# Kernel optimization log

Measured on AMD Instinct MI355X. Metric: run time of the kernel, lower is better.

## Reference

```python
import jax, jax.numpy as jnp
import numpy as np
from functools import partial

B, DIN, H, D, HW = 4096, 2048, 1024, 256, 256
MAX_STEPS = 15
STEP = 1.0 / MAX_STEPS
WEIGHT = 1.0


def safe_norm(x):
    # per-sample L2 norm, keepdims, nan-safe at 0
    return jnp.sqrt(jnp.sum(x * x, axis=-1, keepdims=True) + 1e-24)


def setup_inputs() -> dict:
    key = jax.random.key(0)
    ks = jax.random.split(key, 16)
    s = lambda fan: 1.0 / np.sqrt(fan)
    inp = {
        'x_start': jax.random.normal(ks[0], (B, DIN), jnp.float32),
        'x_end': jax.random.normal(ks[1], (B, DIN), jnp.float32),
        'noise_raw': jax.random.normal(ks[2], (B, D), jnp.float32),
        # encoder params
        'W1': jax.random.normal(ks[3], (DIN, H), jnp.float32) * s(DIN),
        'b1': jnp.zeros((H,), jnp.float32),
        'W2': jax.random.normal(ks[4], (H, D), jnp.float32) * s(H),
        'b2': jnp.zeros((D,), jnp.float32),
        # Zermelo wind field params
        'Ww1': jax.random.normal(ks[5], (D, HW), jnp.float32) * s(D),
        'bw1': jnp.zeros((HW,), jnp.float32),
        'Ww2': jax.random.normal(ks[6], (HW, D), jnp.float32) * s(HW),
        'bw2': jnp.zeros((D,), jnp.float32),
        # conformal potential phi params (metric g = exp(phi) I)
        'Wp1': jax.random.normal(ks[7], (D, HW), jnp.float32) * s(D),
        'bp1': jnp.zeros((HW,), jnp.float32),
        'wp2': jax.random.normal(ks[8], (HW,), jnp.float32) * s(HW),
    }
    return inp


def _encode(x, W1, b1, W2, b2):
    return jnp.tanh(x @ W1 + b1) @ W2 + b2  # [B, D]


def _wind(z, Ww1, bw1, Ww2, bw2):
    return jnp.tanh(z @ Ww1 + bw1) @ Ww2 + bw2  # [B, D]


def _grad_phi(x, Wp1, bp1, wp2):
    # phi(x) = wp2 . tanh(x @ Wp1 + bp1); analytic gradient, fully vectorized
    h = jnp.tanh(x @ Wp1 + bp1)          # [B, HW]
    return ((1.0 - h * h) * wp2) @ Wp1.T  # [B, D]


def _accel(x, v, Wp1, bp1, wp2):
    # geodesic spray of conformal metric e^{phi} I:
    # a = -(grad_phi . v) v + 0.5 |v|^2 grad_phi
    g = _grad_phi(x, Wp1, bp1, wp2)
    gv = jnp.sum(g * v, axis=-1, keepdims=True)
    vv = jnp.sum(v * v, axis=-1, keepdims=True)
    return -gv * v + 0.5 * vv * g


def _trace(z0, v0, Wp1, bp1, wp2):
    h = STEP
    acc = partial(_accel, Wp1=Wp1, bp1=bp1, wp2=wp2)

    def step(carry, _):
        x, v = carry
        k1x, k1v = v, acc(x, v)
        k2x, k2v = v + 0.5 * h * k1v, acc(x + 0.5 * h * k1x, v + 0.5 * h * k1v)
        k3x, k3v = v + 0.5 * h * k2v, acc(x + 0.5 * h * k2x, v + 0.5 * h * k2v)
        k4x, k4v = v + h * k3v, acc(x + h * k3x, v + h * k3v)
        xn = x + (h / 6.0) * (k1x + 2 * k2x + 2 * k3x + k4x)
        vn = v + (h / 6.0) * (k1v + 2 * k2v + 2 * k3v + k4v)
        return (xn, vn), xn

    (_, _), xs = jax.lax.scan(step, (z0, v0), None, length=MAX_STEPS)
    return xs  # [MAX_STEPS, B, D] == xs[1:] of the original trace


def reference(x_start, x_end, noise_raw, W1, b1, W2, b2,
              Ww1, bw1, Ww2, bw2, Wp1, bp1, wp2):
    z_s = _encode(x_start, W1, b1, W2, b2)
    z_e = _encode(x_end, W1, b1, W2, b2)
    W_start = _wind(z_s, Ww1, bw1, Ww2, bw2)
    # degenerate-wind fallback: tiny tangent noise (Euclidean manifold -> identity projection)
    noise = noise_raw / (safe_norm(noise_raw) + 1e-12) * 1e-4
    w_norm = safe_norm(W_start)  # [B, 1]
    W_start = jnp.where(w_norm < 1e-5, W_start + noise, W_start)
    xs = _trace(z_s, W_start, Wp1, bp1, wp2)          # [S, B, D]
    dists_sq = jnp.sum((xs - z_e) ** 2, axis=-1)      # [S, B]
    min_dist_sq = jnp.min(dists_sq, axis=0)           # closest approach per sample
    return jnp.mean(min_dist_sq) * WEIGHT
```

## Files before the change

kernel.cpp:

```cpp
#include <hip/hip_runtime.h>
#include <math.h>

typedef short bf8 __attribute__((ext_vector_type(8)));
typedef float f32x4 __attribute__((ext_vector_type(4)));

namespace {

constexpr float H_STEP = 1.0f / 15.0f;

__device__ inline short f2bf(float f) {
  unsigned u = __float_as_uint(f);
  u += 0x7fffu + ((u >> 16) & 1u);
  return (short)(u >> 16);
}

__device__ inline float fast_tanh(float x) {
  const float ax = fabsf(x);
  const float e = __expf(-2.0f * ax);
  const float t = (1.0f - e) * __builtin_amdgcn_rcpf(1.0f + e);
  return copysignf(t, x);
}

__device__ inline float sech2(float x) {
  const float e = __expf(-2.0f * fabsf(x));
  const float r = __builtin_amdgcn_rcpf(1.0f + e);
  return 4.0f * e * r * r;
}

__device__ inline float wave_sum(float v) {
#pragma unroll
  for (int sh = 32; sh > 0; sh >>= 1) v += __shfl_xor(v, sh);
  return v;
}

template <int CTRL>
__device__ inline float dppadd(float v) {
  return v + __int_as_float(__builtin_amdgcn_update_dpp(
                 0, __float_as_int(v), CTRL, 0xF, 0xF, true));
}
__device__ inline float red16(float v) {
  v = dppadd<0x121>(v);
  v = dppadd<0x122>(v);
  v = dppadd<0x124>(v);
  v = dppadd<0x128>(v);
  return v;
}

__device__ inline void async16(const void* g, void* l) {
  __builtin_amdgcn_global_load_lds((__attribute__((address_space(1))) void*)g,
                                   (__attribute__((address_space(3))) void*)l,
                                   16, 0, 0);
}


__global__ __launch_bounds__(256) void cvt2(const float* __restrict__ a,
                                            const float* __restrict__ b,
                                            short* __restrict__ dst, long n) {
  const long half = n >> 1;
  long i = ((long)blockIdx.x * 256 + threadIdx.x) * 4;
  const long stride = (long)gridDim.x * 1024;
  for (; i < n; i += stride) {
    const float* s = (i < half) ? (a + i) : (b + (i - half));
    const float4 f = *(const float4*)s;
    ushort4 o;
    o.x = (unsigned short)f2bf(f.x);
    o.y = (unsigned short)f2bf(f.y);
    o.z = (unsigned short)f2bf(f.z);
    o.w = (unsigned short)f2bf(f.w);
    *(ushort4*)(dst + i) = o;
  }
}

__global__ __launch_bounds__(256) void cvt_w(
    const float* __restrict__ W1, const float* __restrict__ W2,
    const float* __restrict__ Ww1, const float* __restrict__ Ww2,
    const float* __restrict__ Wp1, const float* __restrict__ wp2,
    short* __restrict__ W1T, short* __restrict__ W2T,
    short* __restrict__ Ww1T, short* __restrict__ Ww2T,
    short* __restrict__ WpT, short* __restrict__ Wp1s) {
  __shared__ float tile[32][33];
  const int id = blockIdx.x;
  const int tr = threadIdx.x >> 5, tc = threadIdx.x & 31;
  const float* src;
  short* dst;
  int K, N, kt, nt;
  if (id < 2048) {
    src = W1; dst = W1T; K = 2048; N = 1024; kt = id >> 5; nt = id & 31;
  } else if (id < 2304) {
    src = W2; dst = W2T; K = 1024; N = 256; kt = (id - 2048) >> 3; nt = (id - 2048) & 7;
  } else if (id < 2368) {
    src = Ww1; dst = Ww1T; K = 256; N = 256; kt = (id - 2304) >> 3; nt = (id - 2304) & 7;
  } else if (id < 2432) {
    src = Ww2; dst = Ww2T; K = 256; N = 256; kt = (id - 2368) >> 3; nt = (id - 2368) & 7;
  } else if (id < 2496) {
    src = Wp1; dst = WpT; K = 256; N = 256; kt = (id - 2432) >> 3; nt = (id - 2432) & 7;
  } else {
    const int lid = id - 2496;
    const int k0 = (lid >> 3) * 32, n0 = (lid & 7) * 32;
#pragma unroll
    for (int i = 0; i < 32; i += 8) {
      const size_t o = (size_t)(k0 + tr + i) * 256 + n0 + tc;
      Wp1s[o] = f2bf(Wp1[o] * wp2[n0 + tc]);
    }
    return;
  }
  const int k0 = kt * 32, n0 = nt * 32;
#pragma unroll
  for (int i = 0; i < 32; i += 8)
    tile[tr + i][tc] = src[(size_t)(k0 + tr + i) * N + n0 + tc];
  __syncthreads();
#pragma unroll
  for (int i = 0; i < 32; i += 8)
    dst[(size_t)(n0 + tr + i) * K + k0 + tc] = f2bf(tile[tc][tr + i]);
}


__global__ __launch_bounds__(256) void gemm128_tanh(
    const short* __restrict__ A, const short* __restrict__ Bt,
    const float* __restrict__ bias, short* __restrict__ Cb, int M, int N,
    int K) {
  __shared__ __align__(16) short As[2 * 128 * 32];
  __shared__ __align__(16) short Bs[2 * 128 * 32];
  const int tid = threadIdx.x;
  const int w = tid >> 6, lane = tid & 63, q = lane >> 4, l15 = lane & 15;
  const int wm = (w >> 1) * 64, wn = (w & 1) * 64;
  const int m0 = blockIdx.y * 128, n0 = blockIdx.x * 128;
  const f32x4 fzero = {0.0f, 0.0f, 0.0f, 0.0f};
  f32x4 acc[4][4];
#pragma unroll
  for (int mt = 0; mt < 4; ++mt)
#pragma unroll
    for (int nt = 0; nt < 4; ++nt) acc[mt][nt] = fzero;

  for (int k0 = 0; k0 < K; k0 += 64) {
#pragma unroll
    for (int kcb = 0; kcb < 2; ++kcb)
#pragma unroll
      for (int j = 0; j < 2; ++j) {
        const int c = w * 128 + j * 64 + lane;
        async16(A + (size_t)(m0 + (c >> 2)) * K + k0 + kcb * 32 + (c & 3) * 8,
                &As[kcb * 4096 + (w * 128 + j * 64) * 8]);
        async16(Bt + (size_t)(n0 + (c >> 2)) * K + k0 + kcb * 32 + (c & 3) * 8,
                &Bs[kcb * 4096 + (w * 128 + j * 64) * 8]);
      }
    __syncthreads();
#pragma unroll
    for (int kcb = 0; kcb < 2; ++kcb) {
      bf8 af[4], bfr[4];
#pragma unroll
      for (int mt = 0; mt < 4; ++mt)
        af[mt] =
            *(const bf8*)&As[kcb * 4096 + (wm + mt * 16 + l15) * 32 + q * 8];
#pragma unroll
      for (int nt = 0; nt < 4; ++nt)
        bfr[nt] =
            *(const bf8*)&Bs[kcb * 4096 + (wn + nt * 16 + l15) * 32 + q * 8];
#pragma unroll
      for (int mt = 0; mt < 4; ++mt)
#pragma unroll
        for (int nt = 0; nt < 4; ++nt)
          acc[mt][nt] = __builtin_amdgcn_mfma_f32_16x16x32_bf16(
              af[mt], bfr[nt], acc[mt][nt], 0, 0, 0);
    }
    __syncthreads();
  }
#pragma unroll
  for (int mt = 0; mt < 4; ++mt)
#pragma unroll
    for (int nt = 0; nt < 4; ++nt) {
      const int col = n0 + wn + nt * 16 + l15;
      const float bcol = bias[col];
#pragma unroll
      for (int rg = 0; rg < 4; ++rg) {
        const int row = m0 + wm + mt * 16 + q * 4 + rg;
        Cb[(size_t)row * N + col] = f2bf(fast_tanh(acc[mt][nt][rg] + bcol));
      }
    }
}

__global__ __launch_bounds__(256) void gemm64_enc2(
    const short* __restrict__ A, const short* __restrict__ Bt,
    const float* __restrict__ bias, float* __restrict__ Zs,
    float* __restrict__ Ze, int M, int N, int K) {
  __shared__ __align__(16) short As[64 * 32];
  __shared__ __align__(16) short Bs[64 * 32];
  const int tid = threadIdx.x;
  const int w = tid >> 6, lane = tid & 63, q = lane >> 4, l15 = lane & 15;
  const int wm = (w >> 1) * 32, wn = (w & 1) * 32;
  const int m0 = blockIdx.y * 64, n0 = blockIdx.x * 64;
  const f32x4 fzero = {0.0f, 0.0f, 0.0f, 0.0f};
  f32x4 acc[2][2];
#pragma unroll
  for (int mt = 0; mt < 2; ++mt)
#pragma unroll
    for (int nt = 0; nt < 2; ++nt) acc[mt][nt] = fzero;

  for (int k0 = 0; k0 < K; k0 += 32) {
    const int c = w * 64 + lane;
    async16(A + (size_t)(m0 + (c >> 2)) * K + k0 + (c & 3) * 8,
            &As[(w * 64) * 8]);
    async16(Bt + (size_t)(n0 + (c >> 2)) * K + k0 + (c & 3) * 8,
            &Bs[(w * 64) * 8]);
    __syncthreads();
    bf8 af[2], bfr[2];
#pragma unroll
    for (int mt = 0; mt < 2; ++mt)
      af[mt] = *(const bf8*)&As[(wm + mt * 16 + l15) * 32 + q * 8];
#pragma unroll
    for (int nt = 0; nt < 2; ++nt)
      bfr[nt] = *(const bf8*)&Bs[(wn + nt * 16 + l15) * 32 + q * 8];
#pragma unroll
    for (int mt = 0; mt < 2; ++mt)
#pragma unroll
      for (int nt = 0; nt < 2; ++nt)
        acc[mt][nt] = __builtin_amdgcn_mfma_f32_16x16x32_bf16(
            af[mt], bfr[nt], acc[mt][nt], 0, 0, 0);
    __syncthreads();
  }
#pragma unroll
  for (int mt = 0; mt < 2; ++mt)
#pragma unroll
    for (int nt = 0; nt < 2; ++nt) {
      const int col = n0 + wn + nt * 16 + l15;
      const float bcol = bias[col];
#pragma unroll
      for (int rg = 0; rg < 4; ++rg) {
        const int row = m0 + wm + mt * 16 + q * 4 + rg;
        const float val = acc[mt][nt][rg] + bcol;
        if (row < 4096)
          Zs[(size_t)row * N + col] = val;
        else
          Ze[(size_t)(row - 4096) * N + col] = val;
      }
    }
}


__global__ __launch_bounds__(512, 2) void trace_fused(
    const float* __restrict__ Xg, const float* __restrict__ ZEg,
    const float* __restrict__ NZg, const short* __restrict__ WT,
    const short* __restrict__ Wp1s, const short* __restrict__ Ww1T,
    const short* __restrict__ Ww2T, const float* __restrict__ bw1,
    const float* __restrict__ bw2, const float* __restrict__ bp1,
    float* __restrict__ out) {
  constexpr float hs = H_STEP;
  __shared__ __align__(16) short XsL[4096];
  __shared__ __align__(16) short UL[4096];
  __shared__ __align__(16) float gvb[2][16];
  __shared__ __align__(16) float vvb[2][16];
  __shared__ __align__(16) float db[2][16];
  const int tid = threadIdx.x;
  const int w = tid >> 6, lane = tid & 63, q = lane >> 4, l15 = lane & 15;
  const int r0 = blockIdx.x * 16, rb = q * 4;

  if (tid < 16) {
    gvb[0][tid] = 0.0f; gvb[1][tid] = 0.0f;
    vvb[0][tid] = 0.0f; vvb[1][tid] = 0.0f;
    db[0][tid] = 0.0f;  db[1][tid] = 0.0f;
  }

  int cc[2], wadr[2][4], radr[8];
  float bp1c[2], bw1c[2], bw2c[2];
#pragma unroll
  for (int t = 0; t < 2; ++t) {
    const int c = w * 32 + t * 16 + l15;
    cc[t] = c;
    const int kc = c >> 3, cx = kc & 15, cl = c & 7;
#pragma unroll
    for (int rg = 0; rg < 4; ++rg)
      wadr[t][rg] = kc * 128 + ((rb + rg) ^ cx) * 8 + cl;
    bp1c[t] = bp1[c];
    bw1c[t] = bw1[c];
    bw2c[t] = bw2[c];
  }
#pragma unroll
  for (int ks = 0; ks < 8; ++ks) {
    const int kq = ks * 4 + q;
    radr[ks] = (kq * 16 + (l15 ^ (kq & 15))) * 8;
  }
  float x[2][4], ze[2][4], nz[2][4];
#pragma unroll
  for (int t = 0; t < 2; ++t)
#pragma unroll
    for (int rg = 0; rg < 4; ++rg) {
      const size_t off = (size_t)(r0 + rb + rg) * 256 + cc[t];
      x[t][rg] = Xg[off];
      ze[t][rg] = ZEg[off];
      nz[t][rg] = NZg[off];
    }
  const f32x4 fzero = {0.0f, 0.0f, 0.0f, 0.0f};

  float v[2][4];
  {
    bf8 Wf1[2][8], Wf2[2][8];
#pragma unroll
    for (int t = 0; t < 2; ++t)
#pragma unroll
      for (int ks = 0; ks < 8; ++ks) {
        Wf1[t][ks] = *(const bf8*)(Ww1T + cc[t] * 256 + ks * 32 + q * 8);
        Wf2[t][ks] = *(const bf8*)(Ww2T + cc[t] * 256 + ks * 32 + q * 8);
      }
#pragma unroll
    for (int t = 0; t < 2; ++t)
#pragma unroll
      for (int rg = 0; rg < 4; ++rg) XsL[wadr[t][rg]] = f2bf(x[t][rg]);
    __syncthreads();
    bf8 af[8];
#pragma unroll
    for (int ks = 0; ks < 8; ++ks) af[ks] = *(const bf8*)&XsL[radr[ks]];
    f32x4 acc[2];
#pragma unroll
    for (int t = 0; t < 2; ++t) {
      f32x4 a0 = fzero, a1 = fzero;
#pragma unroll
      for (int ks = 0; ks < 8; ks += 2) {
        a0 = __builtin_amdgcn_mfma_f32_16x16x32_bf16(af[ks], Wf1[t][ks], a0,
                                                     0, 0, 0);
        a1 = __builtin_amdgcn_mfma_f32_16x16x32_bf16(af[ks + 1],
                                                     Wf1[t][ks + 1], a1, 0, 0,
                                                     0);
      }
      acc[t] = a0 + a1;
    }
#pragma unroll
    for (int t = 0; t < 2; ++t)
#pragma unroll
      for (int rg = 0; rg < 4; ++rg)
        UL[wadr[t][rg]] = f2bf(fast_tanh(acc[t][rg] + bw1c[t]));
    __syncthreads();
#pragma unroll
    for (int ks = 0; ks < 8; ++ks) af[ks] = *(const bf8*)&UL[radr[ks]];
#pragma unroll
    for (int t = 0; t < 2; ++t) {
      f32x4 a0 = fzero, a1 = fzero;
#pragma unroll
      for (int ks = 0; ks < 8; ks += 2) {
        a0 = __builtin_amdgcn_mfma_f32_16x16x32_bf16(af[ks], Wf2[t][ks], a0,
                                                     0, 0, 0);
        a1 = __builtin_amdgcn_mfma_f32_16x16x32_bf16(af[ks + 1],
                                                     Wf2[t][ks + 1], a1, 0, 0,
                                                     0);
      }
      acc[t] = a0 + a1;
#pragma unroll
      for (int rg = 0; rg < 4; ++rg) v[t][rg] = acc[t][rg] + bw2c[t];
    }
    float pn[4], pm[4];
#pragma unroll
    for (int rg = 0; rg < 4; ++rg) {
      pn[rg] = red16(v[0][rg] * v[0][rg] + v[1][rg] * v[1][rg]);
      pm[rg] = red16(nz[0][rg] * nz[0][rg] + nz[1][rg] * nz[1][rg]);
    }
    if (l15 == 0) {
#pragma unroll
      for (int rg = 0; rg < 4; ++rg) {
        atomicAdd(&gvb[0][rb + rg], pn[rg]);
        atomicAdd(&vvb[0][rb + rg], pm[rg]);
      }
    }
    __syncthreads();
#pragma unroll
    for (int rg = 0; rg < 4; ++rg) {
      const float wn = sqrtf(gvb[0][rb + rg] + 1e-24f);
      const float sc = (wn < 1e-5f)
                           ? 1e-4f / (sqrtf(vvb[0][rb + rg] + 1e-24f) + 1e-12f)
                           : 0.0f;
      v[0][rg] = fmaf(sc, nz[0][rg], v[0][rg]);
      v[1][rg] = fmaf(sc, nz[1][rg], v[1][rg]);
    }
    __syncthreads();
    if (tid < 16) {
      gvb[0][tid] = 0.0f;
      vvb[0][tid] = 0.0f;
    }
  }

  bf8 B1f[2][8], B2f[2][8];
#pragma unroll
  for (int t = 0; t < 2; ++t)
#pragma unroll
    for (int ks = 0; ks < 8; ++ks) {
      B1f[t][ks] = *(const bf8*)(WT + cc[t] * 256 + ks * 32 + q * 8);
      B2f[t][ks] = *(const bf8*)(Wp1s + cc[t] * 256 + ks * 32 + q * 8);
    }
  float ap[2][4], xacc[2][4], vacc[2][4], md[4];
#pragma unroll
  for (int rg = 0; rg < 4; ++rg) {
    ap[0][rg] = 0.0f; ap[1][rg] = 0.0f;
    xacc[0][rg] = 0.0f; xacc[1][rg] = 0.0f;
    vacc[0][rg] = 0.0f; vacc[1][rg] = 0.0f;
    md[rg] = 3.4e38f;
  }
  const float cxv_t[4] = {0.0f, 0.5f * hs, 0.5f * hs, hs};
  const float cxa_t[4] = {0.0f, 0.0f, 0.25f * hs * hs, 0.5f * hs * hs};
  const float cva_t[4] = {0.0f, 0.5f * hs, 0.5f * hs, hs};

#pragma unroll 1
  for (int step = 0; step < 15; ++step) {
#pragma unroll
    for (int st = 0; st < 4; ++st) {
      const int p = st & 1;
      const float cxv = cxv_t[st], cxa = cxa_t[st], cva = cva_t[st];
#pragma unroll
      for (int t = 0; t < 2; ++t)
#pragma unroll
        for (int rg = 0; rg < 4; ++rg)
          XsL[wadr[t][rg]] =
              f2bf(x[t][rg] + cxv * v[t][rg] + cxa * ap[t][rg]);
      __syncthreads();
      bf8 af[8];
#pragma unroll
      for (int ks = 0; ks < 8; ++ks) af[ks] = *(const bf8*)&XsL[radr[ks]];
      f32x4 acc[2];
#pragma unroll
      for (int t = 0; t < 2; ++t) {
        f32x4 a0 = fzero, a1 = fzero;
#pragma unroll
        for (int ks = 0; ks < 8; ks += 2) {
          a0 = __builtin_amdgcn_mfma_f32_16x16x32_bf16(af[ks], B1f[t][ks], a0,
                                                       0, 0, 0);
          a1 = __builtin_amdgcn_mfma_f32_16x16x32_bf16(af[ks + 1],
                                                       B1f[t][ks + 1], a1, 0,
                                                       0, 0);
        }
        acc[t] = a0 + a1;
      }
#pragma unroll
      for (int t = 0; t < 2; ++t)
#pragma unroll
        for (int rg = 0; rg < 4; ++rg)
          UL[wadr[t][rg]] = f2bf(sech2(acc[t][rg] + bp1c[t]));
      if (tid < 16) {
        gvb[p ^ 1][tid] = 0.0f;
        vvb[p ^ 1][tid] = 0.0f;
      }
      __syncthreads();
#pragma unroll
      for (int ks = 0; ks < 8; ++ks) af[ks] = *(const bf8*)&UL[radr[ks]];
#pragma unroll
      for (int t = 0; t < 2; ++t) {
        f32x4 a0 = fzero, a1 = fzero;
#pragma unroll
        for (int ks = 0; ks < 8; ks += 2) {
          a0 = __builtin_amdgcn_mfma_f32_16x16x32_bf16(af[ks], B2f[t][ks], a0,
                                                       0, 0, 0);
          a1 = __builtin_amdgcn_mfma_f32_16x16x32_bf16(af[ks + 1],
                                                       B2f[t][ks + 1], a1, 0,
                                                       0, 0);
        }
        acc[t] = a0 + a1;
      }
      float vs[2][4], pg[4], pv[4];
#pragma unroll
      for (int rg = 0; rg < 4; ++rg) {
        vs[0][rg] = fmaf(cva, ap[0][rg], v[0][rg]);
        vs[1][rg] = fmaf(cva, ap[1][rg], v[1][rg]);
        pg[rg] = red16(fmaf(acc[0][rg], vs[0][rg], acc[1][rg] * vs[1][rg]));
        pv[rg] = red16(fmaf(vs[0][rg], vs[0][rg], vs[1][rg] * vs[1][rg]));
      }
      if (l15 == 0) {
#pragma unroll
        for (int rg = 0; rg < 4; ++rg) {
          atomicAdd(&gvb[p][rb + rg], pg[rg]);
          atomicAdd(&vvb[p][rb + rg], pv[rg]);
        }
      }
      __syncthreads();
      const f32x4 gv4 = *(const f32x4*)&gvb[p][rb];
      const f32x4 vv4 = *(const f32x4*)&vvb[p][rb];
#pragma unroll
      for (int t = 0; t < 2; ++t)
#pragma unroll
        for (int rg = 0; rg < 4; ++rg) {
          const float a = -gv4[rg] * vs[t][rg] + 0.5f * vv4[rg] * acc[t][rg];
          ap[t][rg] = a;
          if (st == 0) {
            xacc[t][rg] = a;
            vacc[t][rg] = a;
          } else if (st < 3) {
            xacc[t][rg] += a;
            vacc[t][rg] += 2.0f * a;
          } else {
            vacc[t][rg] += a;
          }
        }
      if (st == 3) {
        const int sp = step & 1;
        float pd[4];
#pragma unroll
        for (int rg = 0; rg < 4; ++rg) {
          float acc_d = 0.0f;
#pragma unroll
          for (int t = 0; t < 2; ++t) {
            const float xn =
                x[t][rg] + hs * v[t][rg] + (hs * hs / 6.0f) * xacc[t][rg];
            const float vn = v[t][rg] + (hs / 6.0f) * vacc[t][rg];
            x[t][rg] = xn;
            v[t][rg] = vn;
            const float d = xn - ze[t][rg];
            acc_d = fmaf(d, d, acc_d);
          }
          pd[rg] = red16(acc_d);
        }
        if (l15 == 0) {
#pragma unroll
          for (int rg = 0; rg < 4; ++rg) atomicAdd(&db[sp][rb + rg], pd[rg]);
        }
        if (tid < 16) db[sp ^ 1][tid] = 0.0f;
        __syncthreads();
        const f32x4 d4 = *(const f32x4*)&db[sp][rb];
#pragma unroll
        for (int rg = 0; rg < 4; ++rg) md[rg] = fminf(md[rg], d4[rg]);
      }
    }
  }
  if (w == 0 && l15 == 0)
    atomicAdd(out, (md[0] + md[1] + md[2] + md[3]) * (1.0f / 4096.0f));
}

}

extern "C" void kernel_launch(void* const* d_in, const int* in_sizes, int n_in,
                              void* d_out, int out_size, void* d_ws,
                              size_t ws_size, hipStream_t stream) {
  (void)in_sizes; (void)n_in; (void)out_size; (void)ws_size;
  const float* x_start = (const float*)d_in[0];
  const float* x_end = (const float*)d_in[1];
  const float* noise = (const float*)d_in[2];
  const float* W1 = (const float*)d_in[3];
  const float* b1 = (const float*)d_in[4];
  const float* W2 = (const float*)d_in[5];
  const float* b2 = (const float*)d_in[6];
  const float* Ww1 = (const float*)d_in[7];
  const float* bw1 = (const float*)d_in[8];
  const float* Ww2 = (const float*)d_in[9];
  const float* bw2 = (const float*)d_in[10];
  const float* Wp1 = (const float*)d_in[11];
  const float* bp1 = (const float*)d_in[12];
  const float* wp2 = (const float*)d_in[13];
  float* out = (float*)d_out;

  float* Xf = (float*)d_ws;
  float* ZEf = Xf + (size_t)4096 * 256;
  short* XSb = (short*)(ZEf + (size_t)4096 * 256);
  short* H1b = XSb + (size_t)8192 * 2048;
  short* W1T = H1b + (size_t)8192 * 1024;
  short* W2T = W1T + (size_t)1024 * 2048;
  short* Ww1T = W2T + (size_t)256 * 1024;
  short* Ww2T = Ww1T + 65536;
  short* WpT = Ww2T + 65536;
  short* Wp1s = WpT + 65536;

  const dim3 blk(256);

  cvt_w<<<2560, blk, 0, stream>>>(W1, W2, Ww1, Ww2, Wp1, wp2, W1T, W2T, Ww1T,
                                  Ww2T, WpT, Wp1s);
  cvt2<<<2048, blk, 0, stream>>>(x_start, x_end, XSb, (long)8192 * 2048);
  gemm128_tanh<<<dim3(8, 64), blk, 0, stream>>>(XSb, W1T, b1, H1b, 8192, 1024,
                                                2048);
  gemm64_enc2<<<dim3(4, 128), blk, 0, stream>>>(H1b, W2T, b2, Xf, ZEf, 8192,
                                                256, 1024);
  hipMemsetAsync(d_out, 0, sizeof(float), stream);
  trace_fused<<<256, dim3(512), 0, stream>>>(Xf, ZEf, noise, WpT, Wp1s, Ww1T,
                                             Ww2T, bw1, bw2, bp1, out);
}
```

Before: 325.5 us.

## Merge prep kernels, deepen enc2 K-step, and cut barriers in trace loop

Folds the input bf16 conversion and weight transpose kernels into one launch to drop a kernel boundary. The second encoder GEMM now loads 64-wide K chunks per barrier pair, halving its synchronisations. In the fused trace kernel, the |v|^2 reduction moves before the first barrier of each stage, and the per-step min-distance read is deferred to the next step's existing barrier. This removes one __syncthreads per RK step, at the cost of more LDS use and subtler buffer-reuse ordering.

```diff
diff --git a/kernel.cpp b/kernel.cpp
--- a/kernel.cpp
+++ b/kernel.cpp
@@ -52,50 +52,48 @@
                                    16, 0, 0);
 }
 
-
-__global__ __launch_bounds__(256) void cvt2(const float* __restrict__ a,
-                                            const float* __restrict__ b,
-                                            short* __restrict__ dst, long n) {
-  const long half = n >> 1;
-  long i = ((long)blockIdx.x * 256 + threadIdx.x) * 4;
-  const long stride = (long)gridDim.x * 1024;
-  for (; i < n; i += stride) {
-    const float* s = (i < half) ? (a + i) : (b + (i - half));
-    const float4 f = *(const float4*)s;
-    ushort4 o;
-    o.x = (unsigned short)f2bf(f.x);
-    o.y = (unsigned short)f2bf(f.y);
-    o.z = (unsigned short)f2bf(f.z);
-    o.w = (unsigned short)f2bf(f.w);
-    *(ushort4*)(dst + i) = o;
-  }
-}
-
-__global__ __launch_bounds__(256) void cvt_w(
+__global__ __launch_bounds__(256) void prep_all(
+    const float* __restrict__ xs, const float* __restrict__ xe,
     const float* __restrict__ W1, const float* __restrict__ W2,
     const float* __restrict__ Ww1, const float* __restrict__ Ww2,
     const float* __restrict__ Wp1, const float* __restrict__ wp2,
-    short* __restrict__ W1T, short* __restrict__ W2T,
+    short* __restrict__ XSb, short* __restrict__ W1T, short* __restrict__ W2T,
     short* __restrict__ Ww1T, short* __restrict__ Ww2T,
     short* __restrict__ WpT, short* __restrict__ Wp1s) {
   __shared__ float tile[32][33];
   const int id = blockIdx.x;
+  if (id < 2048) {
+    const long n = (long)8192 * 2048, half = n >> 1;
+    long i = ((long)id * 256 + threadIdx.x) * 4;
+    const long stride = (long)2048 * 1024;
+    for (; i < n; i += stride) {
+      const float* s = (i < half) ? (xs + i) : (xe + (i - half));
+      const float4 f = *(const float4*)s;
+      ushort4 o;
+      o.x = (unsigned short)f2bf(f.x);
+      o.y = (unsigned short)f2bf(f.y);
+      o.z = (unsigned short)f2bf(f.z);
+      o.w = (unsigned short)f2bf(f.w);
+      *(ushort4*)(XSb + i) = o;
+    }
+    return;
+  }
   const int tr = threadIdx.x >> 5, tc = threadIdx.x & 31;
   const float* src;
   short* dst;
   int K, N, kt, nt;
-  if (id < 2048) {
-    src = W1; dst = W1T; K = 2048; N = 1024; kt = id >> 5; nt = id & 31;
-  } else if (id < 2304) {
-    src = W2; dst = W2T; K = 1024; N = 256; kt = (id - 2048) >> 3; nt = (id - 2048) & 7;
-  } else if (id < 2368) {
-    src = Ww1; dst = Ww1T; K = 256; N = 256; kt = (id - 2304) >> 3; nt = (id - 2304) & 7;
-  } else if (id < 2432) {
-    src = Ww2; dst = Ww2T; K = 256; N = 256; kt = (id - 2368) >> 3; nt = (id - 2368) & 7;
-  } else if (id < 2496) {
-    src = Wp1; dst = WpT; K = 256; N = 256; kt = (id - 2432) >> 3; nt = (id - 2432) & 7;
+  if (id < 4096) {
+    src = W1; dst = W1T; K = 2048; N = 1024; kt = (id - 2048) >> 5; nt = (id - 2048) & 31;
+  } else if (id < 4352) {
+    src = W2; dst = W2T; K = 1024; N = 256; kt = (id - 4096) >> 3; nt = (id - 4096) & 7;
+  } else if (id < 4416) {
+    src = Ww1; dst = Ww1T; K = 256; N = 256; kt = (id - 4352) >> 3; nt = (id - 4352) & 7;
+  } else if (id < 4480) {
+    src = Ww2; dst = Ww2T; K = 256; N = 256; kt = (id - 4416) >> 3; nt = (id - 4416) & 7;
+  } else if (id < 4544) {
+    src = Wp1; dst = WpT; K = 256; N = 256; kt = (id - 4480) >> 3; nt = (id - 4480) & 7;
   } else {
-    const int lid = id - 2496;
+    const int lid = id - 4544;
     const int k0 = (lid >> 3) * 32, n0 = (lid & 7) * 32;
 #pragma unroll
     for (int i = 0; i < 32; i += 8) {
@@ -182,8 +180,8 @@
     const short* __restrict__ A, const short* __restrict__ Bt,
     const float* __restrict__ bias, float* __restrict__ Zs,
     float* __restrict__ Ze, int M, int N, int K) {
-  __shared__ __align__(16) short As[64 * 32];
-  __shared__ __align__(16) short Bs[64 * 32];
+  __shared__ __align__(16) short As[2 * 64 * 32];
+  __shared__ __align__(16) short Bs[2 * 64 * 32];
   const int tid = threadIdx.x;
   const int w = tid >> 6, lane = tid & 63, q = lane >> 4, l15 = lane & 15;
   const int wm = (w >> 1) * 32, wn = (w & 1) * 32;
@@ -195,26 +193,34 @@
 #pragma unroll
     for (int nt = 0; nt < 2; ++nt) acc[mt][nt] = fzero;
 
-  for (int k0 = 0; k0 < K; k0 += 32) {
+  for (int k0 = 0; k0 < K; k0 += 64) {
     const int c = w * 64 + lane;
-    async16(A + (size_t)(m0 + (c >> 2)) * K + k0 + (c & 3) * 8,
-            &As[(w * 64) * 8]);
-    async16(Bt + (size_t)(n0 + (c >> 2)) * K + k0 + (c & 3) * 8,
-            &Bs[(w * 64) * 8]);
-    __syncthreads();
-    bf8 af[2], bfr[2];
-#pragma unroll
-    for (int mt = 0; mt < 2; ++mt)
-      af[mt] = *(const bf8*)&As[(wm + mt * 16 + l15) * 32 + q * 8];
-#pragma unroll
-    for (int nt = 0; nt < 2; ++nt)
-      bfr[nt] = *(const bf8*)&Bs[(wn + nt * 16 + l15) * 32 + q * 8];
-#pragma unroll
-    for (int mt = 0; mt < 2; ++mt)
+#pragma unroll
+    for (int kcb = 0; kcb < 2; ++kcb) {
+      async16(A + (size_t)(m0 + (c >> 2)) * K + k0 + kcb * 32 + (c & 3) * 8,
+              &As[kcb * 2048 + (w * 64) * 8]);
+      async16(Bt + (size_t)(n0 + (c >> 2)) * K + k0 + kcb * 32 + (c & 3) * 8,
+              &Bs[kcb * 2048 + (w * 64) * 8]);
+    }
+    __syncthreads();
+#pragma unroll
+    for (int kcb = 0; kcb < 2; ++kcb) {
+      bf8 af[2], bfr[2];
+#pragma unroll
+      for (int mt = 0; mt < 2; ++mt)
+        af[mt] =
+            *(const bf8*)&As[kcb * 2048 + (wm + mt * 16 + l15) * 32 + q * 8];
 #pragma unroll
       for (int nt = 0; nt < 2; ++nt)
-        acc[mt][nt] = __builtin_amdgcn_mfma_f32_16x16x32_bf16(
-            af[mt], bfr[nt], acc[mt][nt], 0, 0, 0);
+        bfr[nt] =
+            *(const bf8*)&Bs[kcb * 2048 + (wn + nt * 16 + l15) * 32 + q * 8];
+#pragma unroll
+      for (int mt = 0; mt < 2; ++mt)
+#pragma unroll
+        for (int nt = 0; nt < 2; ++nt)
+          acc[mt][nt] = __builtin_amdgcn_mfma_f32_16x16x32_bf16(
+              af[mt], bfr[nt], acc[mt][nt], 0, 0, 0);
+    }
     __syncthreads();
   }
 #pragma unroll
@@ -373,6 +379,7 @@
       gvb[0][tid] = 0.0f;
       vvb[0][tid] = 0.0f;
     }
+    __syncthreads();
   }
 
   bf8 B1f[2][8], B2f[2][8];
@@ -401,13 +408,31 @@
     for (int st = 0; st < 4; ++st) {
       const int p = st & 1;
       const float cxv = cxv_t[st], cxa = cxa_t[st], cva = cva_t[st];
+      float vs[2][4];
 #pragma unroll
       for (int t = 0; t < 2; ++t)
 #pragma unroll
-        for (int rg = 0; rg < 4; ++rg)
+        for (int rg = 0; rg < 4; ++rg) {
+          vs[t][rg] = fmaf(cva, ap[t][rg], v[t][rg]);
           XsL[wadr[t][rg]] =
               f2bf(x[t][rg] + cxv * v[t][rg] + cxa * ap[t][rg]);
+        }
+      {
+        float pv[4];
+#pragma unroll
+        for (int rg = 0; rg < 4; ++rg)
+          pv[rg] = red16(fmaf(vs[0][rg], vs[0][rg], vs[1][rg] * vs[1][rg]));
+        if (l15 == 0) {
+#pragma unroll
+          for (int rg = 0; rg < 4; ++rg) atomicAdd(&vvb[p][rb + rg], pv[rg]);
+        }
+      }
       __syncthreads();
+      if (st == 0 && step > 0) {
+        const f32x4 d4 = *(const f32x4*)&db[(step - 1) & 1][rb];
+#pragma unroll
+        for (int rg = 0; rg < 4; ++rg) md[rg] = fminf(md[rg], d4[rg]);
+      }
       bf8 af[8];
 #pragma unroll
       for (int ks = 0; ks < 8; ++ks) af[ks] = *(const bf8*)&XsL[radr[ks]];
@@ -435,6 +460,7 @@
         vvb[p ^ 1][tid] = 0.0f;
       }
       __syncthreads();
+      if (st == 0 && step > 0 && tid < 16) db[(step - 1) & 1][tid] = 0.0f;
 #pragma unroll
       for (int ks = 0; ks < 8; ++ks) af[ks] = *(const bf8*)&UL[radr[ks]];
 #pragma unroll
@@ -450,19 +476,15 @@
         }
         acc[t] = a0 + a1;
       }
-      float vs[2][4], pg[4], pv[4];
-#pragma unroll
-      for (int rg = 0; rg < 4; ++rg) {
-        vs[0][rg] = fmaf(cva, ap[0][rg], v[0][rg]);
-        vs[1][rg] = fmaf(cva, ap[1][rg], v[1][rg]);
-        pg[rg] = red16(fmaf(acc[0][rg], vs[0][rg], acc[1][rg] * vs[1][rg]));
-        pv[rg] = red16(fmaf(vs[0][rg], vs[0][rg], vs[1][rg] * vs[1][rg]));
-      }
-      if (l15 == 0) {
-#pragma unroll
-        for (int rg = 0; rg < 4; ++rg) {
-          atomicAdd(&gvb[p][rb + rg], pg[rg]);
-          atomicAdd(&vvb[p][rb + rg], pv[rg]);
+      {
+        float pg[4];
+#pragma unroll
+        for (int rg = 0; rg < 4; ++rg)
+          pg[rg] =
+              red16(fmaf(acc[0][rg], vs[0][rg], acc[1][rg] * vs[1][rg]));
+        if (l15 == 0) {
+#pragma unroll
+          for (int rg = 0; rg < 4; ++rg) atomicAdd(&gvb[p][rb + rg], pg[rg]);
         }
       }
       __syncthreads();
@@ -506,13 +528,14 @@
 #pragma unroll
           for (int rg = 0; rg < 4; ++rg) atomicAdd(&db[sp][rb + rg], pd[rg]);
         }
-        if (tid < 16) db[sp ^ 1][tid] = 0.0f;
-        __syncthreads();
-        const f32x4 d4 = *(const f32x4*)&db[sp][rb];
-#pragma unroll
-        for (int rg = 0; rg < 4; ++rg) md[rg] = fminf(md[rg], d4[rg]);
-      }
-    }
+      }
+    }
+  }
+  __syncthreads();
+  {
+    const f32x4 d4 = *(const f32x4*)&db[14 & 1][rb];
+#pragma unroll
+    for (int rg = 0; rg < 4; ++rg) md[rg] = fminf(md[rg], d4[rg]);
   }
   if (w == 0 && l15 == 0)
     atomicAdd(out, (md[0] + md[1] + md[2] + md[3]) * (1.0f / 4096.0f));
@@ -553,9 +576,9 @@
 
   const dim3 blk(256);
 
-  cvt_w<<<2560, blk, 0, stream>>>(W1, W2, Ww1, Ww2, Wp1, wp2, W1T, W2T, Ww1T,
-                                  Ww2T, WpT, Wp1s);
-  cvt2<<<2048, blk, 0, stream>>>(x_start, x_end, XSb, (long)8192 * 2048);
+  prep_all<<<4608, blk, 0, stream>>>(x_start, x_end, W1, W2, Ww1, Ww2, Wp1,
+                                     wp2, XSb, W1T, W2T, Ww1T, Ww2T, WpT,
+                                     Wp1s);
   gemm128_tanh<<<dim3(8, 64), blk, 0, stream>>>(XSb, W1T, b1, H1b, 8192, 1024,
                                                 2048);
   gemm64_enc2<<<dim3(4, 128), blk, 0, stream>>>(H1b, W2T, b2, Xf, ZEf, 8192,
```

Result: no change. 325.2 us (-0.1%).
